# Kernel tuning notes

Measured on AMD Instinct MI355X. Metric: run time of the kernel, lower is better.

The kernel has to match this reference:

```python
import jax, jax.numpy as jnp
import numpy as np

EMBED = 1024
HEADS = 16
HEAD_DIM = EMBED // HEADS


def setup_inputs() -> dict:
    key = jax.random.key(0)
    ks = jax.random.split(key, 12)
    B, S, E = 2, 2048, EMBED
    scale = 1.0 / np.sqrt(E)
    inp = {
        "query": jax.random.normal(ks[0], (B, S, E), jnp.float32),
        "key": jax.random.normal(ks[1], (B, S, E), jnp.float32),
        "value": jax.random.normal(ks[2], (B, S, E), jnp.float32),
        "Wq": jax.random.normal(ks[3], (E, E), jnp.float32) * scale,
        "bq": jax.random.normal(ks[4], (E,), jnp.float32) * 0.01,
        "Wk": jax.random.normal(ks[5], (E, E), jnp.float32) * scale,
        "bk": jax.random.normal(ks[6], (E,), jnp.float32) * 0.01,
        "Wv": jax.random.normal(ks[7], (E, E), jnp.float32) * scale,
        "bv": jax.random.normal(ks[8], (E,), jnp.float32) * 0.01,
        "Wo": jax.random.normal(ks[9], (E, E), jnp.float32) * scale,
        "bo": jax.random.normal(ks[10], (E,), jnp.float32) * 0.01,
    }
    return inp


def reference(query, key, value, Wq, bq, Wk, bk, Wv, bv, Wo, bo):
    B, Sq, E = query.shape
    Sk = key.shape[1]
    H, D = HEADS, HEAD_DIM
    # QKV projections (torch Linear: x @ W.T + b)
    q = (query @ Wq.T + bq).reshape(B, Sq, H, D)
    k = (key @ Wk.T + bk).reshape(B, Sk, H, D)
    v = (value @ Wv.T + bv).reshape(B, Sk, H, D)
    # energy: [B, H, Sq, Sk]; note scale = 1/sqrt(embed_size), not head_dim
    energy = jnp.einsum("bqhd,bkhd->bhqk", q, k)
    scale = jnp.asarray(E, energy.dtype) ** 0.5
    attn = jax.nn.softmax(energy / scale, axis=-1)
    out = jnp.einsum("bhqk,bkhd->bqhd", attn, v).reshape(B, Sq, E)
    # fc_out (dropout is identity at eval)
    return out @ Wo.T + bo
```

## Files before the change

### kernel.cpp

```cpp
#include <hip/hip_runtime.h>
#include <hip/hip_bf16.h>

typedef __hip_bfloat16 bf16;
typedef short frag8 __attribute__((ext_vector_type(8)));
typedef _Float16 half4 __attribute__((ext_vector_type(4)));
typedef _Float16 half8 __attribute__((ext_vector_type(8)));
typedef __fp16 fp16x2 __attribute__((ext_vector_type(2)));
typedef float f32x4 __attribute__((ext_vector_type(4)));

typedef __attribute__((address_space(3))) void lds_void;
typedef __attribute__((address_space(1))) const void gbl_void;

__device__ __forceinline__ void gld16(const void* g, void* l) {
  __builtin_amdgcn_global_load_lds((gbl_void*)g, (lds_void*)l, 16, 0, 0);
}

__device__ __forceinline__ unsigned short f2bf(float f) {
  union { float f; unsigned u; } x; x.f = f;
  unsigned r = x.u + 0x7FFFu + ((x.u >> 16) & 1u);
  return (unsigned short)(r >> 16);
}

#define QSCALE 0.0450842200278f
#define MFIX 4.0f

struct CvtArgs {
  const float4* src[7];
  ushort4* dst[7];
  int n4[7];
};
__global__ __launch_bounds__(256) void cvt_all(CvtArgs a) {
  const int t = blockIdx.y;
  const int i = blockIdx.x * 256 + threadIdx.x;
  if (i >= a.n4[t]) return;
  float4 v = a.src[t][i];
  ushort4 o;
  o.x = f2bf(v.x); o.y = f2bf(v.y); o.z = f2bf(v.z); o.w = f2bf(v.w);
  a.dst[t][i] = o;
}

__device__ __forceinline__ void mfma32(f32x4 (&acc)[8][4], const frag8 (&a8)[8], const frag8 (&b4)[4]) {
  __builtin_amdgcn_s_setprio(1);
  #pragma unroll
  for (int i = 0; i < 8; ++i) {
    #pragma unroll
    for (int j = 0; j < 4; ++j)
      acc[i][j] = __builtin_amdgcn_mfma_f32_16x16x32_bf16(a8[i], b4[j], acc[i][j], 0, 0, 0);
  }
  __builtin_amdgcn_s_setprio(0);
}

__global__ __launch_bounds__(512, 2)
void gemm_qkv256(const bf16* __restrict__ A0, const bf16* __restrict__ A1, const bf16* __restrict__ A2,
                 const bf16* __restrict__ W0, const bf16* __restrict__ W1, const bf16* __restrict__ W2,
                 const float* __restrict__ b0, const float* __restrict__ b1, const float* __restrict__ b2,
                 void* __restrict__ o0, void* __restrict__ o1, void* __restrict__ o2) {
  __shared__ __align__(16) char smem[131072];
  bf16* As = (bf16*)smem;
  bf16* Bs = (bf16*)(smem + 65536);
  const int tid = threadIdx.x;
  const int wave = tid >> 6, lane = tid & 63, quad = lane >> 4, l16 = lane & 15;
  const int wm = wave >> 2, wn = wave & 3;
  const int bn = blockIdx.x, bm = blockIdx.y, z = blockIdx.z;

  const bf16* A = A0; const bf16* W = W0; const float* bias = b0; void* out = o0;
  if (z == 1) { A = A1; W = W1; bias = b1; out = o1; }
  else if (z == 2) { A = A2; W = W2; bias = b2; out = o2; }

  const bf16* Ab = A + (size_t)bm * 256 * 1024;
  const bf16* Wb = W + (size_t)bn * 256 * 1024;
  const int c0_ = tid & 3, r0_ = tid >> 2;
  const int gcp = ((c0_ ^ ((r0_ >> 1) & 3)) << 3);
  const int rc2 = (quad ^ ((l16 >> 1) & 3)) << 3;

  auto stageA = [&](int kt, bf16* dst) {
    #pragma unroll
    for (int is = 0; is < 2; ++is) {
      const int r = r0_ + is * 128;
      gld16(Ab + (size_t)r * 1024 + kt * 32 + gcp, (void*)(dst + (is * 512 + tid) * 8));
    }
  };
  auto stageW = [&](int kt, bf16* dst) {
    #pragma unroll
    for (int is = 0; is < 2; ++is) {
      const int r = r0_ + is * 128;
      gld16(Wb + (size_t)r * 1024 + kt * 32 + gcp, (void*)(dst + (is * 512 + tid) * 8));
    }
  };
  auto ldsA8 = [&](const bf16* ah, frag8 (&a8)[8]) {
    #pragma unroll
    for (int i = 0; i < 8; ++i)
      a8[i] = *(const frag8*)&ah[(wm * 128 + i * 16 + l16) * 32 + rc2];
  };
  auto ldsB4 = [&](const bf16* bh, frag8 (&b4)[4]) {
    #pragma unroll
    for (int j = 0; j < 4; ++j)
      b4[j] = *(const frag8*)&bh[(wn * 64 + j * 16 + l16) * 32 + rc2];
  };

  f32x4 acc[8][4];
  #pragma unroll
  for (int i = 0; i < 8; ++i)
    #pragma unroll
    for (int j = 0; j < 4; ++j)
      acc[i][j] = (f32x4){0.f, 0.f, 0.f, 0.f};

  stageA(0, As + 0 * 8192); stageW(0, Bs + 0 * 8192);
  stageA(1, As + 1 * 8192); stageW(1, Bs + 1 * 8192);
  stageA(2, As + 2 * 8192); stageW(2, Bs + 2 * 8192);

  #pragma unroll 4
  for (int t = 0; t < 28; ++t) {
    asm volatile("s_waitcnt vmcnt(8)" ::: "memory");
    __builtin_amdgcn_s_barrier();
    const bf16* ab = As + (t & 3) * 8192;
    const bf16* bb = Bs + (t & 3) * 8192;
    frag8 a8[8], b4[4];
    ldsA8(ab, a8); ldsB4(bb, b4);
    stageA(t + 3, As + ((t + 3) & 3) * 8192);
    stageW(t + 3, Bs + ((t + 3) & 3) * 8192);
    asm volatile("s_waitcnt lgkmcnt(0)" ::: "memory");
    mfma32(acc, a8, b4);
  }
  {
    asm volatile("s_waitcnt vmcnt(8)" ::: "memory");
    __builtin_amdgcn_s_barrier();
    frag8 a8[8], b4[4];
    ldsA8(As + 0 * 8192, a8); ldsB4(Bs + 0 * 8192, b4);
    stageA(31, As + 3 * 8192);
    stageW(31, Bs + 3 * 8192);
    asm volatile("s_waitcnt lgkmcnt(0)" ::: "memory");
    mfma32(acc, a8, b4);
  }
  {
    asm volatile("s_waitcnt vmcnt(8)" ::: "memory");
    __builtin_amdgcn_s_barrier();
    frag8 a8[8], b4[4];
    ldsA8(As + 1 * 8192, a8); ldsB4(Bs + 1 * 8192, b4);
    asm volatile("s_waitcnt lgkmcnt(0)" ::: "memory");
    mfma32(acc, a8, b4);
  }
  {
    asm volatile("s_waitcnt vmcnt(4)" ::: "memory");
    __builtin_amdgcn_s_barrier();
    frag8 a8[8], b4[4];
    ldsA8(As + 2 * 8192, a8); ldsB4(Bs + 2 * 8192, b4);
    asm volatile("s_waitcnt lgkmcnt(0)" ::: "memory");
    mfma32(acc, a8, b4);
  }
  {
    asm volatile("s_waitcnt vmcnt(0)" ::: "memory");
    __builtin_amdgcn_s_barrier();
    frag8 a8[8], b4[4];
    ldsA8(As + 3 * 8192, a8); ldsB4(Bs + 3 * 8192, b4);
    asm volatile("s_waitcnt lgkmcnt(0)" ::: "memory");
    mfma32(acc, a8, b4);
  }

  if (z == 2) {
    _Float16* vlds = (_Float16*)smem;
    __builtin_amdgcn_s_barrier();
    #pragma unroll
    for (int j = 0; j < 4; ++j) {
      const int col = bn * 256 + wn * 64 + j * 16 + l16;
      const float bv = bias[col];
      const int d = j * 16 + l16;
      #pragma unroll
      for (int i = 0; i < 8; ++i) {
        const int g = wm * 2 + (i >> 2);
        const int kb = (i & 3) * 16 + quad * 4;
        half4 h;
        #pragma unroll
        for (int r = 0; r < 4; ++r)
          h[r] = (_Float16)(acc[i][j][r] + bv);
        const int off = ((wn * 4 + g) << 12) + d * 64 + ((((kb >> 3) ^ (d & 7)) << 3)) + (kb & 7);
        *(half4*)&vlds[off] = h;
      }
    }
    __builtin_amdgcn_s_barrier();
    const int b_ = bm >> 3;
    #pragma unroll
    for (int rd = 0; rd < 16; ++rd) {
      const int l = rd * 4096 + tid * 8;
      const int wnp = l >> 14, g = (l >> 12) & 3, off = l & 4095;
      const size_t bhp = (size_t)(b_ * 16 + bn * 4 + wnp);
      const size_t addr = bhp * 131072 + (size_t)((bm & 7) * 4 + g) * 4096 + (size_t)off;
      *(uint4*)&((_Float16*)out)[addr] = *(const uint4*)&vlds[l];
    }
  } else {
    #pragma unroll
    for (int j = 0; j < 4; ++j) {
      const int col = bn * 256 + wn * 64 + j * 16 + l16;
      const float bv = bias[col];
      #pragma unroll
      for (int i = 0; i < 8; ++i) {
        #pragma unroll
        for (int r = 0; r < 4; ++r) {
          const int row = bm * 256 + wm * 128 + i * 16 + quad * 4 + r;
          float v = acc[i][j][r] + bv;
          const int b = row >> 11, s = row & 2047;
          const int hh = col >> 6, d = col & 63;
          const size_t bh = (size_t)(b * 16 + hh);
          if (z == 0) {
            v *= QSCALE;
            ((bf16*)out)[(bh * 2048 + s) * 64 + d] = __float2bfloat16(v);
          } else {
            const int g = s >> 6, l32 = s & 31, G32 = (s >> 5) & 1;
            const int q_ = (l32 >> 3) & 3, t_ = (l32 >> 2) & 1, i_ = l32 & 3;
            const int r64 = G32 * 32 + t_ * 16 + q_ * 4 + i_;
            const size_t addr = bh * 131072 + (size_t)g * 4096 + (size_t)r64 * 64
                              + (size_t)(((d >> 3) ^ (r64 & 7)) << 3) + (d & 7);
            ((bf16*)out)[addr] = __float2bfloat16(v);
          }
        }
      }
    }
  }
}

__global__ __launch_bounds__(256, 3)
void gemm_out(const bf16* __restrict__ A, const bf16* __restrict__ W,
              const float* __restrict__ bias, float* __restrict__ out) {
  __shared__ __align__(16) char smem[49152];
  bf16* As = (bf16*)smem;
  bf16* Bs = (bf16*)(smem + 32768);
  const int tid = threadIdx.x;
  const int wave = tid >> 6, lane = tid & 63, quad = lane >> 4, l16 = lane & 15;
  const int wm = wave >> 1, wn = wave & 1;
  const int bn = blockIdx.x, bm = blockIdx.y;

  const bf16* Ab = A + (size_t)bm * 128 * 1024;
  const bf16* Wb = W + (size_t)bn * 64 * 1024;
  const int c0_ = tid & 3, r0_ = tid >> 2;
  const int gcp = ((c0_ ^ ((r0_ >> 1) & 3)) << 3);
  const int rc2 = (quad ^ ((l16 >> 1) & 3)) << 3;

  auto stageA = [&](int kt, bf16* dst) {
    #pragma unroll
    for (int is = 0; is < 2; ++is) {
      const int r = r0_ + is * 64;
      gld16(Ab + (size_t)r * 1024 + kt * 32 + gcp, (void*)(dst + (is * 256 + tid) * 8));
    }
  };
  auto stageW = [&](int kt, bf16* dst) {
    gld16(Wb + (size_t)r0_ * 1024 + kt * 32 + gcp, (void*)(dst + tid * 8));
  };
  auto ldsA4 = [&](const bf16* ah, frag8 (&a4)[4]) {
    #pragma unroll
    for (int i = 0; i < 4; ++i)
      a4[i] = *(const frag8*)&ah[(wm * 64 + i * 16 + l16) * 32 + rc2];
  };
  auto ldsB2 = [&](const bf16* bh, frag8 (&b2)[2]) {
    #pragma unroll
    for (int j = 0; j < 2; ++j)
      b2[j] = *(const frag8*)&bh[(wn * 32 + j * 16 + l16) * 32 + rc2];
  };

  f32x4 acc[4][2];
  #pragma unroll
  for (int i = 0; i < 4; ++i)
    #pragma unroll
    for (int j = 0; j < 2; ++j)
      acc[i][j] = (f32x4){0.f, 0.f, 0.f, 0.f};

  stageA(0, As + 0 * 4096); stageW(0, Bs + 0 * 2048);
  stageA(1, As + 1 * 4096); stageW(1, Bs + 1 * 2048);
  stageA(2, As + 2 * 4096); stageW(2, Bs + 2 * 2048);

  auto body = [&](const bf16* ab, const bf16* bb) {
    frag8 a4[4], b2[2];
    ldsA4(ab, a4); ldsB2(bb, b2);
    asm volatile("s_waitcnt lgkmcnt(0)" ::: "memory");
    __builtin_amdgcn_s_setprio(1);
    #pragma unroll
    for (int i = 0; i < 4; ++i)
      #pragma unroll
      for (int j = 0; j < 2; ++j)
        acc[i][j] = __builtin_amdgcn_mfma_f32_16x16x32_bf16(a4[i], b2[j], acc[i][j], 0, 0, 0);
    __builtin_amdgcn_s_setprio(0);
  };

  #pragma unroll 4
  for (int t = 0; t < 29; ++t) {
    asm volatile("s_waitcnt vmcnt(6)" ::: "memory");
    __builtin_amdgcn_s_barrier();
    const bf16* ab = As + (t & 3) * 4096;
    const bf16* bb = Bs + (t & 3) * 2048;
    frag8 a4[4], b2[2];
    ldsA4(ab, a4); ldsB2(bb, b2);
    stageA(t + 3, As + ((t + 3) & 3) * 4096);
    stageW(t + 3, Bs + ((t + 3) & 3) * 2048);
    asm volatile("s_waitcnt lgkmcnt(0)" ::: "memory");
    __builtin_amdgcn_s_setprio(1);
    #pragma unroll
    for (int i = 0; i < 4; ++i)
      #pragma unroll
      for (int j = 0; j < 2; ++j)
        acc[i][j] = __builtin_amdgcn_mfma_f32_16x16x32_bf16(a4[i], b2[j], acc[i][j], 0, 0, 0);
    __builtin_amdgcn_s_setprio(0);
  }
  {
    asm volatile("s_waitcnt vmcnt(6)" ::: "memory");
    __builtin_amdgcn_s_barrier();
    body(As + 1 * 4096, Bs + 1 * 2048);
  }
  {
    asm volatile("s_waitcnt vmcnt(3)" ::: "memory");
    __builtin_amdgcn_s_barrier();
    body(As + 2 * 4096, Bs + 2 * 2048);
  }
  {
    asm volatile("s_waitcnt vmcnt(0)" ::: "memory");
    __builtin_amdgcn_s_barrier();
    body(As + 3 * 4096, Bs + 3 * 2048);
  }

  #pragma unroll
  for (int j = 0; j < 2; ++j) {
    const int col = bn * 64 + wn * 32 + j * 16 + l16;
    const float bv = bias[col];
    #pragma unroll
    for (int i = 0; i < 4; ++i) {
      #pragma unroll
      for (int r = 0; r < 4; ++r) {
        const int row = bm * 128 + wm * 64 + i * 16 + quad * 4 + r;
        out[(size_t)row * 1024 + col] = acc[i][j][r] + bv;
      }
    }
  }
}

__global__ __launch_bounds__(512, 2)
void flash_attn(const bf16* __restrict__ Q, const bf16* __restrict__ K,
                const _Float16* __restrict__ Vt, bf16* __restrict__ ctx) {
  __shared__ __align__(16) char smem[65536];
  bf16* Ks = (bf16*)smem;
  _Float16* Vs = (_Float16*)(smem + 32768);
  const int tid = threadIdx.x;
  const int wave = tid >> 6, lane = tid & 63, quad = lane >> 4, l16 = lane & 15;
  const int qg = wave & 3, kvg = wave >> 2;
  const int bh = blockIdx.x, b = bh >> 4, h = bh & 15;
  const int q0 = blockIdx.y * 256 + qg * 64;
  const bf16* Qb = Q + (size_t)bh * 131072;
  const bf16* Kb = K + (size_t)bh * 131072;
  const _Float16* Vb = Vt + (size_t)bh * 131072;

  frag8 qf[4][2];
  #pragma unroll
  for (int qt = 0; qt < 4; ++qt)
    #pragma unroll
    for (int ks = 0; ks < 2; ++ks)
      qf[qt][ks] = *(const frag8*)(Qb + (size_t)(q0 + qt * 16 + l16) * 64 + ks * 32 + quad * 8);

  f32x4 rsv[4];
  f32x4 o[4][4];
  #pragma unroll
  for (int qt = 0; qt < 4; ++qt) {
    rsv[qt] = (f32x4){0.f, 0.f, 0.f, 0.f};
    #pragma unroll
    for (int dt = 0; dt < 4; ++dt)
      o[qt][dt] = (f32x4){0.f, 0.f, 0.f, 0.f};
  }

  const int xk = l16 & 7;

  auto stage = [&](int kt, int buf) {
    #pragma unroll
    for (int s = 0; s < 2; ++s) {
      const int g = s * 16 + kt;
      gld16(Kb + (size_t)g * 4096 + (size_t)tid * 8, (void*)(Ks + (s * 2 + buf) * 4096 + tid * 8));
      gld16(Vb + (size_t)g * 4096 + (size_t)tid * 8, (void*)(Vs + (s * 2 + buf) * 4096 + tid * 8));
    }
  };

  stage(0, 0);
  #pragma unroll 2
  for (int kt = 0; kt < 16; ++kt) {
    __syncthreads();
    if (kt < 15) stage(kt + 1, (kt + 1) & 1);
    const bf16* ks_ = Ks + (kvg * 2 + (kt & 1)) * 4096;
    const _Float16* vs_ = Vs + (kvg * 2 + (kt & 1)) * 4096;

    f32x4 s[4][4];
    #pragma unroll
    for (int qt = 0; qt < 4; ++qt)
      #pragma unroll
      for (int jt = 0; jt < 4; ++jt)
        s[qt][jt] = (f32x4){-MFIX, -MFIX, -MFIX, -MFIX};
    #pragma unroll
    for (int ks = 0; ks < 2; ++ks) {
      frag8 kf[4];
      #pragma unroll
      for (int jt = 0; jt < 4; ++jt)
        kf[jt] = *(const frag8*)&ks_[(jt * 16 + l16) * 64 + (((ks * 4 + quad) ^ xk) << 3)];
      __builtin_amdgcn_s_setprio(1);
      #pragma unroll
      for (int qt = 0; qt < 4; ++qt)
        #pragma unroll
        for (int jt = 0; jt < 4; ++jt)
          s[qt][jt] = __builtin_amdgcn_mfma_f32_16x16x32_bf16(kf[jt], qf[qt][ks], s[qt][jt], 0, 0, 0);
      __builtin_amdgcn_s_setprio(0);
    }

    half8 pb[4][2];
    #pragma unroll
    for (int qt = 0; qt < 4; ++qt) {
      #pragma unroll
      for (int jt = 0; jt < 4; ++jt) {
        f32x4 p4;
        #pragma unroll
        for (int r = 0; r < 4; ++r)
          p4[r] = __builtin_amdgcn_exp2f(s[qt][jt][r]);
        rsv[qt] += p4;
        union { fp16x2 h2[2]; half4 h4; } u;
        u.h2[0] = __builtin_amdgcn_cvt_pkrtz(p4[0], p4[1]);
        u.h2[1] = __builtin_amdgcn_cvt_pkrtz(p4[2], p4[3]);
        const int jtp = jt >> 1, hi = (jt & 1) * 4;
        pb[qt][jtp][hi + 0] = u.h4[0];
        pb[qt][jtp][hi + 1] = u.h4[1];
        pb[qt][jtp][hi + 2] = u.h4[2];
        pb[qt][jtp][hi + 3] = u.h4[3];
      }
    }

    #pragma unroll
    for (int jtp = 0; jtp < 2; ++jtp) {
      half8 vf[4];
      #pragma unroll
      for (int dt = 0; dt < 4; ++dt)
        vf[dt] = *(const half8*)&vs_[(dt * 16 + l16) * 64 + (((jtp * 4 + quad) ^ xk) << 3)];
      __builtin_amdgcn_s_setprio(1);
      #pragma unroll
      for (int qt = 0; qt < 4; ++qt)
        #pragma unroll
        for (int dt = 0; dt < 4; ++dt)
          o[qt][dt] = __builtin_amdgcn_mfma_f32_16x16x32_f16(vf[dt], pb[qt][jtp], o[qt][dt], 0, 0, 0);
      __builtin_amdgcn_s_setprio(0);
    }
  }

  float4* mo = (float4*)smem;
  float*  ml = (float*)(smem + 32768);
  const int mbase = (qg * 64 + lane) * 8;
  #pragma unroll
  for (int r = 0; r < 2; ++r) {
    __syncthreads();
    if (kvg == 1) {
      #pragma unroll
      for (int qh = 0; qh < 2; ++qh) {
        const int qt = r * 2 + qh;
        #pragma unroll
        for (int dt = 0; dt < 4; ++dt) {
          const int i = qh * 4 + dt;
          mo[mbase + (i ^ (lane & 7))] = (float4){o[qt][dt][0], o[qt][dt][1], o[qt][dt][2], o[qt][dt][3]};
        }
        ml[(qg * 64 + lane) * 2 + qh] = rsv[qt][0] + rsv[qt][1] + rsv[qt][2] + rsv[qt][3];
      }
    }
    __syncthreads();
    if (kvg == 0) {
      #pragma unroll
      for (int qh = 0; qh < 2; ++qh) {
        const int qt = r * 2 + qh;
        float l = rsv[qt][0] + rsv[qt][1] + rsv[qt][2] + rsv[qt][3]
                + ml[(qg * 64 + lane) * 2 + qh];
        l += __shfl_xor(l, 16, 64);
        l += __shfl_xor(l, 32, 64);
        const float inv = __builtin_amdgcn_rcpf(l);
        const int q = q0 + qt * 16 + l16;
        #pragma unroll
        for (int dt = 0; dt < 4; ++dt) {
          const int i = qh * 4 + dt;
          const float4 po = mo[mbase + (i ^ (lane & 7))];
          ushort4 w;
          w.x = f2bf((o[qt][dt][0] + po.x) * inv);
          w.y = f2bf((o[qt][dt][1] + po.y) * inv);
          w.z = f2bf((o[qt][dt][2] + po.z) * inv);
          w.w = f2bf((o[qt][dt][3] + po.w) * inv);
          const int d = dt * 16 + quad * 4;
          *(uint2*)&ctx[((size_t)(b * 2048 + q)) * 1024 + h * 64 + d] = *(uint2*)&w;
        }
      }
    }
  }
}

extern "C" void kernel_launch(void* const* d_in, const int* in_sizes, int n_in,
                              void* d_out, int out_size, void* d_ws, size_t ws_size,
                              hipStream_t stream) {
  const float* q_in = (const float*)d_in[0];
  const float* k_in = (const float*)d_in[1];
  const float* v_in = (const float*)d_in[2];
  const float* Wq = (const float*)d_in[3];
  const float* bq = (const float*)d_in[4];
  const float* Wk = (const float*)d_in[5];
  const float* bk = (const float*)d_in[6];
  const float* Wv = (const float*)d_in[7];
  const float* bv = (const float*)d_in[8];
  const float* Wo = (const float*)d_in[9];
  const float* bo = (const float*)d_in[10];

  char* ws = (char*)d_ws;
  const size_t MB = 1024 * 1024;
  bf16* Xq  = (bf16*)(ws + 0 * MB);
  bf16* Xk  = (bf16*)(ws + 8 * MB);
  bf16* Xv  = (bf16*)(ws + 16 * MB);
  bf16* Wqb = (bf16*)(ws + 24 * MB);
  bf16* Wkb = (bf16*)(ws + 26 * MB);
  bf16* Wvb = (bf16*)(ws + 28 * MB);
  bf16* Wob = (bf16*)(ws + 30 * MB);
  bf16* Qw  = (bf16*)(ws + 32 * MB);
  bf16* Kw  = (bf16*)(ws + 40 * MB);
  _Float16* Vtw = (_Float16*)(ws + 48 * MB);
  bf16* Ctx = (bf16*)(ws + 56 * MB);

  {
    CvtArgs a;
    a.src[0] = (const float4*)q_in; a.dst[0] = (ushort4*)Xq;  a.n4[0] = 4194304 / 4;
    a.src[1] = (const float4*)k_in; a.dst[1] = (ushort4*)Xk;  a.n4[1] = 4194304 / 4;
    a.src[2] = (const float4*)v_in; a.dst[2] = (ushort4*)Xv;  a.n4[2] = 4194304 / 4;
    a.src[3] = (const float4*)Wq;   a.dst[3] = (ushort4*)Wqb; a.n4[3] = 1048576 / 4;
    a.src[4] = (const float4*)Wk;   a.dst[4] = (ushort4*)Wkb; a.n4[4] = 1048576 / 4;
    a.src[5] = (const float4*)Wv;   a.dst[5] = (ushort4*)Wvb; a.n4[5] = 1048576 / 4;
    a.src[6] = (const float4*)Wo;   a.dst[6] = (ushort4*)Wob; a.n4[6] = 1048576 / 4;
    cvt_all<<<dim3(4096, 7), 256, 0, stream>>>(a);
  }

  gemm_qkv256<<<dim3(4, 16, 3), 512, 0, stream>>>(Xq, Xk, Xv, Wqb, Wkb, Wvb,
                                                  bq, bk, bv, Qw, Kw, (bf16*)Vtw);
  flash_attn<<<dim3(32, 8), 512, 0, stream>>>(Qw, Kw, Vtw, Ctx);
  gemm_out<<<dim3(16, 32), 256, 0, stream>>>(Ctx, Wob, bo, (float*)d_out);
}
```

Baseline: 207.0 us.

## Software-pipeline flash attention to overlap softmax exp with previous tile's PV MFMAs

Restructures the attention inner loop so the PV matmul for tile kt-1 is interleaved with the exp/convert of tile kt's scores, keeping the previous P fragments in registers. To keep V tiles alive one iteration longer, the V buffer grows to a 4-deep ring and shared memory rises from 64KB to 96KB. This aims to hide transcendental and conversion latency behind MFMA work, at the cost of more registers and LDS, which may reduce occupancy below the two blocks per CU the launch bounds request.

```diff
diff --git a/kernel.cpp b/kernel.cpp
--- a/kernel.cpp
+++ b/kernel.cpp
@@ -333,7 +333,7 @@
 __global__ __launch_bounds__(512, 2)
 void flash_attn(const bf16* __restrict__ Q, const bf16* __restrict__ K,
                 const _Float16* __restrict__ Vt, bf16* __restrict__ ctx) {
-  __shared__ __align__(16) char smem[65536];
+  __shared__ __align__(16) char smem[98304];
   bf16* Ks = (bf16*)smem;
   _Float16* Vs = (_Float16*)(smem + 32768);
   const int tid = threadIdx.x;
@@ -364,24 +364,17 @@
 
   const int xk = l16 & 7;
 
-  auto stage = [&](int kt, int buf) {
+  auto stage = [&](int kt) {
     #pragma unroll
     for (int s = 0; s < 2; ++s) {
       const int g = s * 16 + kt;
-      gld16(Kb + (size_t)g * 4096 + (size_t)tid * 8, (void*)(Ks + (s * 2 + buf) * 4096 + tid * 8));
-      gld16(Vb + (size_t)g * 4096 + (size_t)tid * 8, (void*)(Vs + (s * 2 + buf) * 4096 + tid * 8));
-    }
-  };
-
-  stage(0, 0);
-  #pragma unroll 2
-  for (int kt = 0; kt < 16; ++kt) {
-    __syncthreads();
-    if (kt < 15) stage(kt + 1, (kt + 1) & 1);
+      gld16(Kb + (size_t)g * 4096 + (size_t)tid * 8, (void*)(Ks + (s * 2 + (kt & 1)) * 4096 + tid * 8));
+      gld16(Vb + (size_t)g * 4096 + (size_t)tid * 8, (void*)(Vs + (s * 4 + (kt & 3)) * 4096 + tid * 8));
+    }
+  };
+
+  auto qk = [&](int kt, f32x4 (&s)[4][4]) {
     const bf16* ks_ = Ks + (kvg * 2 + (kt & 1)) * 4096;
-    const _Float16* vs_ = Vs + (kvg * 2 + (kt & 1)) * 4096;
-
-    f32x4 s[4][4];
     #pragma unroll
     for (int qt = 0; qt < 4; ++qt)
       #pragma unroll
@@ -401,10 +394,18 @@
           s[qt][jt] = __builtin_amdgcn_mfma_f32_16x16x32_bf16(kf[jt], qf[qt][ks], s[qt][jt], 0, 0, 0);
       __builtin_amdgcn_s_setprio(0);
     }
-
-    half8 pb[4][2];
-    #pragma unroll
-    for (int qt = 0; qt < 4; ++qt) {
+  };
+
+  half8 pbp[4][2];
+  f32x4 s[4][4];
+
+  stage(0);
+  {
+    __syncthreads();
+    stage(1);
+    qk(0, s);
+    #pragma unroll
+    for (int qt = 0; qt < 4; ++qt)
       #pragma unroll
       for (int jt = 0; jt < 4; ++jt) {
         f32x4 p4;
@@ -412,31 +413,79 @@
         for (int r = 0; r < 4; ++r)
           p4[r] = __builtin_amdgcn_exp2f(s[qt][jt][r]);
         rsv[qt] += p4;
-        union { fp16x2 h2[2]; half4 h4; } u;
-        u.h2[0] = __builtin_amdgcn_cvt_pkrtz(p4[0], p4[1]);
-        u.h2[1] = __builtin_amdgcn_cvt_pkrtz(p4[2], p4[3]);
-        const int jtp = jt >> 1, hi = (jt & 1) * 4;
-        pb[qt][jtp][hi + 0] = u.h4[0];
-        pb[qt][jtp][hi + 1] = u.h4[1];
-        pb[qt][jtp][hi + 2] = u.h4[2];
-        pb[qt][jtp][hi + 3] = u.h4[3];
-      }
-    }
-
-    #pragma unroll
-    for (int jtp = 0; jtp < 2; ++jtp) {
-      half8 vf[4];
+        union { fp16x2 h2[2]; half4 h4; } up;
+        up.h2[0] = __builtin_amdgcn_cvt_pkrtz(p4[0], p4[1]);
+        up.h2[1] = __builtin_amdgcn_cvt_pkrtz(p4[2], p4[3]);
+        const int jp = jt >> 1, hi = (jt & 1) * 4;
+        pbp[qt][jp][hi + 0] = up.h4[0];
+        pbp[qt][jp][hi + 1] = up.h4[1];
+        pbp[qt][jp][hi + 2] = up.h4[2];
+        pbp[qt][jp][hi + 3] = up.h4[3];
+      }
+  }
+
+  #pragma unroll 2
+  for (int kt = 1; kt < 16; ++kt) {
+    __syncthreads();
+    if (kt < 15) stage(kt + 1);
+    const _Float16* vsp = Vs + (kvg * 4 + ((kt - 1) & 3)) * 4096;
+    half8 vfp[8];
+    #pragma unroll
+    for (int jtp = 0; jtp < 2; ++jtp)
       #pragma unroll
       for (int dt = 0; dt < 4; ++dt)
-        vf[dt] = *(const half8*)&vs_[(dt * 16 + l16) * 64 + (((jtp * 4 + quad) ^ xk) << 3)];
-      __builtin_amdgcn_s_setprio(1);
+        vfp[jtp * 4 + dt] = *(const half8*)&vsp[(dt * 16 + l16) * 64 + (((jtp * 4 + quad) ^ xk) << 3)];
+
+    qk(kt, s);
+
+    half8 pbc[4][2];
+    #pragma unroll
+    for (int uu = 0; uu < 16; ++uu) {
+      const int qt = uu >> 2, jt = uu & 3;
+      #pragma unroll
+      for (int k2 = 0; k2 < 2; ++k2) {
+        const int m = uu * 2 + k2;
+        const int jtp = m >> 4, rem = m & 15, qq = rem >> 2, dt = rem & 3;
+        o[qq][dt] = __builtin_amdgcn_mfma_f32_16x16x32_f16(vfp[jtp * 4 + dt], pbp[qq][jtp], o[qq][dt], 0, 0, 0);
+      }
+      f32x4 p4;
+      #pragma unroll
+      for (int r = 0; r < 4; ++r)
+        p4[r] = __builtin_amdgcn_exp2f(s[qt][jt][r]);
+      rsv[qt] += p4;
+      union { fp16x2 h2[2]; half4 h4; } up;
+      up.h2[0] = __builtin_amdgcn_cvt_pkrtz(p4[0], p4[1]);
+      up.h2[1] = __builtin_amdgcn_cvt_pkrtz(p4[2], p4[3]);
+      const int jp = jt >> 1, hi = (jt & 1) * 4;
+      pbc[qt][jp][hi + 0] = up.h4[0];
+      pbc[qt][jp][hi + 1] = up.h4[1];
+      pbc[qt][jp][hi + 2] = up.h4[2];
+      pbc[qt][jp][hi + 3] = up.h4[3];
+    }
+    #pragma unroll
+    for (int qt = 0; qt < 4; ++qt)
+      #pragma unroll
+      for (int jp = 0; jp < 2; ++jp)
+        pbp[qt][jp] = pbc[qt][jp];
+  }
+
+  {
+    const _Float16* vsp = Vs + (kvg * 4 + 3) * 4096;
+    half8 vfp[8];
+    #pragma unroll
+    for (int jtp = 0; jtp < 2; ++jtp)
+      #pragma unroll
+      for (int dt = 0; dt < 4; ++dt)
+        vfp[jtp * 4 + dt] = *(const half8*)&vsp[(dt * 16 + l16) * 64 + (((jtp * 4 + quad) ^ xk) << 3)];
+    __builtin_amdgcn_s_setprio(1);
+    #pragma unroll
+    for (int jtp = 0; jtp < 2; ++jtp)
       #pragma unroll
       for (int qt = 0; qt < 4; ++qt)
         #pragma unroll
         for (int dt = 0; dt < 4; ++dt)
-          o[qt][dt] = __builtin_amdgcn_mfma_f32_16x16x32_f16(vf[dt], pb[qt][jtp], o[qt][dt], 0, 0, 0);
-      __builtin_amdgcn_s_setprio(0);
-    }
+          o[qt][dt] = __builtin_amdgcn_mfma_f32_16x16x32_f16(vfp[jtp * 4 + dt], pbp[qt][jtp], o[qt][dt], 0, 0, 0);
+    __builtin_amdgcn_s_setprio(0);
   }
 
   float4* mo = (float4*)smem;
```

After: 454.2 us. +119.4%, slower.
